# Performance work log

Hardware: AMD Instinct MI355X
Metric: run time of the kernel (lower is better)

## Reference

```python
import jax, jax.numpy as jnp
import numpy as np

HEADS = 8
DIM_HEAD = 64
SCALE = DIM_HEAD ** -0.5


def setup_inputs() -> dict:
    key = jax.random.key(0)
    ks = jax.random.split(key, 6)
    B, N, D = 4, 2048, 512
    inner = HEADS * DIM_HEAD  # 512
    x = jax.random.normal(ks[0], (B, N, D), dtype=jnp.float32)
    centroid_delta = jax.random.normal(ks[1], (B, 3, N, N), dtype=jnp.float32)
    Wqkv = jax.random.normal(ks[2], (D, 3 * inner), dtype=jnp.float32) * (D ** -0.5)
    Wout = jax.random.normal(ks[3], (inner, D), dtype=jnp.float32) * (inner ** -0.5)
    bout = jnp.zeros((D,), dtype=jnp.float32)
    rel_w = jax.random.normal(ks[4], (HEADS, 3), dtype=jnp.float32)
    rel_b = jnp.zeros((HEADS,), dtype=jnp.float32)
    return {"x": x, "centroid_delta": centroid_delta, "Wqkv": Wqkv,
            "Wout": Wout, "bout": bout, "rel_w": rel_w, "rel_b": rel_b}


def reference(x, centroid_delta, Wqkv, Wout, bout, rel_w, rel_b):
    B, N, D = x.shape
    h, d = HEADS, DIM_HEAD
    qkv = x @ Wqkv                      # [B, N, 3*h*d]
    q, k, v = jnp.split(qkv, 3, axis=-1)
    # [B, N, h*d] -> [B, h, N, d]
    reshape = lambda t: t.reshape(B, N, h, d).transpose(0, 2, 1, 3)
    q, k, v = reshape(q), reshape(k), reshape(v)
    dots = jnp.einsum('bhid,bhjd->bhij', q, k) * SCALE  # [B, h, N, N]
    # 1x1 conv: Conv2d(3, heads, 1) on centroid_delta [B, 3, N, N]
    bias = jnp.einsum('hc,bcij->bhij', rel_w, centroid_delta) + rel_b[None, :, None, None]
    attn = jax.nn.softmax(dots + bias, axis=-1)
    out = jnp.einsum('bhij,bhjd->bhid', attn, v)        # [B, h, N, d]
    out = out.transpose(0, 2, 1, 3).reshape(B, N, h * d)
    return out @ Wout + bout
```

## Files before the change

kernel.cpp:

```cpp
#include <hip/hip_runtime.h>
#include <hip/hip_bf16.h>

typedef __bf16 bf16_t;
typedef __bf16 bf16x8 __attribute__((ext_vector_type(8)));
typedef float f32x4 __attribute__((ext_vector_type(4)));

#define SCALE_ 0.125f
#define BATCH 4
#define NSEQ 2048
#define DMODEL 512
#define HEADS 8
#define DHEAD 64
#define QKVN 1536
#define NN ((size_t)NSEQ * NSEQ)

#define BAR() asm volatile("s_waitcnt lgkmcnt(0)\n\ts_barrier" ::: "memory")

__device__ __forceinline__ void gload_lds16(const void* g, void* l) {
  __builtin_amdgcn_global_load_lds((const __attribute__((address_space(1))) void*)g,
                                   (__attribute__((address_space(3))) void*)l, 16, 0, 0);
}

__device__ __forceinline__ f32x4 mfma16(bf16x8 a, bf16x8 b, f32x4 c) {
  return __builtin_amdgcn_mfma_f32_16x16x32_bf16(a, b, c, 0, 0, 0);
}

__global__ __launch_bounds__(256) void cvt_bf16_kernel(const float* __restrict__ in,
                                                       bf16_t* __restrict__ out, int n4) {
  int i = blockIdx.x * 256 + threadIdx.x;
  if (i < n4) {
    float4 v = ((const float4*)in)[i];
    union { bf16_t b[4]; uint2 u; } pk;
    pk.b[0] = (bf16_t)v.x; pk.b[1] = (bf16_t)v.y;
    pk.b[2] = (bf16_t)v.z; pk.b[3] = (bf16_t)v.w;
    ((uint2*)out)[i] = pk.u;
  }
}

__global__ __launch_bounds__(256) void cvt_transpose_kernel(const float* __restrict__ in,
                                                            bf16_t* __restrict__ out, int R, int C) {
  __shared__ float tile[64][65];
  const int r0 = blockIdx.y * 64, c0 = blockIdx.x * 64;
  const int tx = threadIdx.x & 63, tg = threadIdx.x >> 6;
#pragma unroll
  for (int i = 0; i < 16; i++) {
    int rr = tg * 16 + i;
    tile[rr][tx] = in[(size_t)(r0 + rr) * C + c0 + tx];
  }
  __syncthreads();
#pragma unroll
  for (int i = 0; i < 16; i++) {
    int cc = tg * 16 + i;
    out[(size_t)(c0 + cc) * R + r0 + tx] = (bf16_t)tile[tx][cc];
  }
}

template<int BIAS, int OUTF32>
__global__ __launch_bounds__(256) void gemm128_kernel(const bf16_t* __restrict__ A,
    const bf16_t* __restrict__ Bt, void* __restrict__ Cout,
    const float* __restrict__ bias, int M, int N, int K) {
  __shared__ __align__(16) bf16_t As[128 * 64];
  __shared__ __align__(16) bf16_t Bs[128 * 64];
  const int tid = threadIdx.x;
  const int w = tid >> 6, lane = tid & 63, quad = lane >> 4, l16 = lane & 15;
  const int wm = w & 1, wn = w >> 1;
  const int m0 = blockIdx.x * 128, n0 = blockIdx.y * 128;
  f32x4 acc[4][4] = {};
  int srow[4], scg[4];
#pragma unroll
  for (int t = 0; t < 4; t++) {
    int s = (w * 4 + t) * 64 + lane;
    srow[t] = s >> 3;
    scg[t] = (s & 7) ^ (srow[t] & 7);
  }
  for (int k0 = 0; k0 < K; k0 += 64) {
#pragma unroll
    for (int t = 0; t < 4; t++) {
      gload_lds16(&A[(size_t)(m0 + srow[t]) * K + k0 + scg[t] * 8], &As[(w * 4 + t) * 512]);
      gload_lds16(&Bt[(size_t)(n0 + srow[t]) * K + k0 + scg[t] * 8], &Bs[(w * 4 + t) * 512]);
    }
    __syncthreads();
    bf16x8 af[4][2], bfr[4][2];
#pragma unroll
    for (int mt = 0; mt < 4; mt++) {
      int row = wm * 64 + mt * 16 + l16;
#pragma unroll
      for (int kh = 0; kh < 2; kh++)
        af[mt][kh] = *(const bf16x8*)&As[(row * 8 + ((kh * 4 + quad) ^ (row & 7))) * 8];
    }
#pragma unroll
    for (int nt = 0; nt < 4; nt++) {
      int row = wn * 64 + nt * 16 + l16;
#pragma unroll
      for (int kh = 0; kh < 2; kh++)
        bfr[nt][kh] = *(const bf16x8*)&Bs[(row * 8 + ((kh * 4 + quad) ^ (row & 7))) * 8];
    }
#pragma unroll
    for (int mt = 0; mt < 4; mt++)
#pragma unroll
      for (int nt = 0; nt < 4; nt++) {
        acc[mt][nt] = mfma16(af[mt][0], bfr[nt][0], acc[mt][nt]);
        acc[mt][nt] = mfma16(af[mt][1], bfr[nt][1], acc[mt][nt]);
      }
    __syncthreads();
  }
#pragma unroll
  for (int nt = 0; nt < 4; nt++) {
    int col = n0 + wn * 64 + nt * 16 + l16;
    float bv = BIAS ? bias[col] : 0.0f;
#pragma unroll
    for (int mt = 0; mt < 4; mt++) {
#pragma unroll
      for (int rr = 0; rr < 4; rr++) {
        int row = m0 + wm * 64 + mt * 16 + quad * 4 + rr;
        float v = acc[mt][nt][rr] + bv;
        if (OUTF32) ((float*)Cout)[(size_t)row * N + col] = v;
        else        ((bf16_t*)Cout)[(size_t)row * N + col] = (bf16_t)v;
      }
    }
  }
}

__global__ __launch_bounds__(256, 4) void attn_kernel(const bf16_t* __restrict__ qkv,
    const float* __restrict__ cd, const float* __restrict__ rel_w,
    const float* __restrict__ rel_b, bf16_t* __restrict__ ao) {
  __shared__ __align__(16) bf16_t Ks[64][72];
  __shared__ __align__(16) bf16_t Vts[64][72];
  __shared__ __align__(16) bf16_t Ps[64][72];
  const int tid = threadIdx.x;
  const int w = tid >> 6, lane = tid & 63, quad = lane >> 4, l16 = lane & 15;
  const int bid = blockIdx.x;
  const int h = bid >> 7, b = (bid >> 5) & 3, it = bid & 31;

  const size_t qoff = (size_t)(b * NSEQ + it * 64 + w * 16 + l16) * QKVN + h * DHEAD;
  bf16x8 q0 = *(const bf16x8*)&qkv[qoff + quad * 8];
  bf16x8 q1 = *(const bf16x8*)&qkv[qoff + 32 + quad * 8];

  const float rw0 = rel_w[h * 3 + 0], rw1 = rel_w[h * 3 + 1], rw2 = rel_w[h * 3 + 2];
  const float rb = rel_b[h];

  f32x4 o[4] = {};
  float m_r[4], l_r[4];
#pragma unroll
  for (int r = 0; r < 4; r++) { m_r[r] = -1e30f; l_r[r] = 0.0f; }

  const int sr = tid >> 3, sg = tid & 7;
  const size_t kbase = (size_t)b * NSEQ * QKVN + DMODEL + h * DHEAD;

  const int row0 = it * 64 + w * 16 + quad * 4;
  const float* cdp = cd + (size_t)b * 3 * NN + (size_t)row0 * NSEQ + l16;
  float biasr[4][4];
#define LOADBIAS(JT) do { const int jb_ = (JT) * 64;                                   \
  _Pragma("unroll") for (int ct_ = 0; ct_ < 4; ct_++)                                  \
  _Pragma("unroll") for (int r_ = 0; r_ < 4; r_++) {                                   \
    size_t ci_ = (size_t)r_ * NSEQ + jb_ + ct_ * 16;                                   \
    biasr[ct_][r_] = fmaf(rw0, cdp[ci_],                                               \
                     fmaf(rw1, cdp[ci_ + NN], fmaf(rw2, cdp[ci_ + 2 * NN], rb)));      \
  } } while (0)

  uint4 k0r, k1r, v0r, v1r;
  {
    const bf16_t* p = &qkv[kbase + (size_t)sr * QKVN + sg * 8];
    k0r = *(const uint4*)p;               v0r = *(const uint4*)(p + DMODEL);
    k1r = *(const uint4*)(p + 32 * QKVN); v1r = *(const uint4*)(p + 32 * QKVN + DMODEL);
  }
  LOADBIAS(0);

  for (int jt = 0; jt < 32; jt++) {
    *(uint4*)&Ks[sr][sg * 8]      = k0r;
    *(uint4*)&Ks[sr + 32][sg * 8] = k1r;
    {
      union { bf16_t e[8]; uint4 u; } va, vb; va.u = v0r; vb.u = v1r;
      const int pc = sr ^ ((sg & 3) << 3);
#pragma unroll
      for (int e2 = 0; e2 < 8; e2++) {
        Vts[sg * 8 + e2][pc]      = va.e[e2];
        Vts[sg * 8 + e2][pc + 32] = vb.e[e2];
      }
    }
    BAR();

    if (jt < 31) {
      const bf16_t* p = &qkv[kbase + (size_t)((jt + 1) * 64 + sr) * QKVN + sg * 8];
      k0r = *(const uint4*)p;               v0r = *(const uint4*)(p + DMODEL);
      k1r = *(const uint4*)(p + 32 * QKVN); v1r = *(const uint4*)(p + 32 * QKVN + DMODEL);
    }

    f32x4 s[4] = {};
#pragma unroll
    for (int ct = 0; ct < 4; ct++) {
      bf16x8 b0 = *(const bf16x8*)&Ks[ct * 16 + l16][quad * 8];
      bf16x8 b1 = *(const bf16x8*)&Ks[ct * 16 + l16][32 + quad * 8];
      s[ct] = mfma16(q0, b0, s[ct]);
      s[ct] = mfma16(q1, b1, s[ct]);
    }

#pragma unroll
    for (int ct = 0; ct < 4; ct++)
#pragma unroll
      for (int r = 0; r < 4; r++)
        s[ct][r] = s[ct][r] * SCALE_ + biasr[ct][r];
    if (jt < 31) LOADBIAS(jt + 1);

#pragma unroll
    for (int r = 0; r < 4; r++) {
      float mx = fmaxf(fmaxf(s[0][r], s[1][r]), fmaxf(s[2][r], s[3][r]));
#pragma unroll
      for (int off = 8; off >= 1; off >>= 1) mx = fmaxf(mx, __shfl_xor(mx, off, 64));
      float mnew = fmaxf(m_r[r], mx);
      float alpha = __expf(m_r[r] - mnew);
      float rsum = 0.0f;
#pragma unroll
      for (int ct = 0; ct < 4; ct++) {
        float p = __expf(s[ct][r] - mnew);
        s[ct][r] = p; rsum += p;
      }
#pragma unroll
      for (int off = 8; off >= 1; off >>= 1) rsum += __shfl_xor(rsum, off, 64);
      l_r[r] = l_r[r] * alpha + rsum;
      m_r[r] = mnew;
#pragma unroll
      for (int dt = 0; dt < 4; dt++) o[dt][r] *= alpha;
    }

#pragma unroll
    for (int ct = 0; ct < 4; ct++)
#pragma unroll
      for (int rr = 0; rr < 4; rr++)
        Ps[w * 16 + quad * 4 + rr][(ct * 16 + l16) ^ (quad << 3)] = (bf16_t)s[ct][rr];

    const int psw = ((l16 >> 2) & 3) << 3;
    bf16x8 p0 = *(const bf16x8*)&Ps[w * 16 + l16][(quad * 8) ^ psw];
    bf16x8 p1 = *(const bf16x8*)&Ps[w * 16 + l16][32 + ((quad * 8) ^ psw)];
#pragma unroll
    for (int dt = 0; dt < 4; dt++) {
      const int row = dt * 16 + l16;
      const int vsw = ((row >> 3) & 3) << 3;
      bf16x8 v0 = *(const bf16x8*)&Vts[row][(quad * 8) ^ vsw];
      bf16x8 v1 = *(const bf16x8*)&Vts[row][32 + ((quad * 8) ^ vsw)];
      o[dt] = mfma16(p0, v0, o[dt]);
      o[dt] = mfma16(p1, v1, o[dt]);
    }
    BAR();
  }

#pragma unroll
  for (int dt = 0; dt < 4; dt++) {
    int col = h * DHEAD + dt * 16 + l16;
#pragma unroll
    for (int rr = 0; rr < 4; rr++) {
      int row = b * NSEQ + it * 64 + w * 16 + quad * 4 + rr;
      ao[(size_t)row * DMODEL + col] = (bf16_t)(o[dt][rr] / l_r[rr]);
    }
  }
#undef LOADBIAS
}

extern "C" void kernel_launch(void* const* d_in, const int* in_sizes, int n_in,
                              void* d_out, int out_size, void* d_ws, size_t ws_size,
                              hipStream_t stream) {
  const float* x     = (const float*)d_in[0];
  const float* cd    = (const float*)d_in[1];
  const float* Wqkv  = (const float*)d_in[2];
  const float* Wout  = (const float*)d_in[3];
  const float* bout  = (const float*)d_in[4];
  const float* rel_w = (const float*)d_in[5];
  const float* rel_b = (const float*)d_in[6];
  float* out = (float*)d_out;

  char* ws = (char*)d_ws;
  const size_t M = (size_t)BATCH * NSEQ;
  bf16_t* xb    = (bf16_t*)ws;
  bf16_t* WqkvT = (bf16_t*)(ws + 8388608);
  bf16_t* WoutT = (bf16_t*)(ws + 8388608 + 1572864);
  bf16_t* qkv   = (bf16_t*)(ws + 8388608 + 1572864 + 524288);
  bf16_t* ao    = (bf16_t*)(ws + 8388608 + 1572864 + 524288 + 25165824);

  cvt_bf16_kernel<<<(int)(M * DMODEL / 4 / 256), 256, 0, stream>>>(x, xb, (int)(M * DMODEL / 4));
  cvt_transpose_kernel<<<dim3(QKVN / 64, DMODEL / 64), 256, 0, stream>>>(Wqkv, WqkvT, DMODEL, QKVN);
  cvt_transpose_kernel<<<dim3(DMODEL / 64, DMODEL / 64), 256, 0, stream>>>(Wout, WoutT, DMODEL, DMODEL);

  gemm128_kernel<0, 0><<<dim3(M / 128, QKVN / 128), 256, 0, stream>>>(
      xb, WqkvT, (void*)qkv, nullptr, (int)M, QKVN, DMODEL);

  attn_kernel<<<BATCH * 32 * HEADS, 256, 0, stream>>>(qkv, cd, rel_w, rel_b, ao);

  gemm128_kernel<1, 1><<<dim3(M / 128, DMODEL / 128), 256, 0, stream>>>(
      ao, WoutT, (void*)out, bout, (int)M, DMODEL, DMODEL);
}
```

Measured before the change: 443.8 us.

## Pre-transpose V, fold softmax scale into Wqkv, deepen centroid-delta prefetch

Adds a separate kernel that writes V transposed per batch-head, so the attention kernel can store V tiles to LDS with plain vector stores instead of scattered scalar transposing writes. The softmax scale is folded into the Q columns of the weight during conversion. Raw centroid-delta values for the next tile are now prefetched into registers and the bias FMA is used as the MFMA accumulator init. Occupancy is lowered to 3 blocks per SM to fit the larger 48-float prefetch buffer. The trade-offs are an extra kernel launch and extra HBM traffic for vT, and lower occupancy in a kernel that is bound by the centroid-delta stream.

```diff
diff --git a/kernel.cpp b/kernel.cpp
--- a/kernel.cpp
+++ b/kernel.cpp
@@ -5,7 +5,6 @@
 typedef __bf16 bf16x8 __attribute__((ext_vector_type(8)));
 typedef float f32x4 __attribute__((ext_vector_type(4)));
 
-#define SCALE_ 0.125f
 #define BATCH 4
 #define NSEQ 2048
 #define DMODEL 512
@@ -15,6 +14,7 @@
 #define NN ((size_t)NSEQ * NSEQ)
 
 #define BAR() asm volatile("s_waitcnt lgkmcnt(0)\n\ts_barrier" ::: "memory")
+#define PIN() asm volatile("" ::: "memory")
 
 __device__ __forceinline__ void gload_lds16(const void* g, void* l) {
   __builtin_amdgcn_global_load_lds((const __attribute__((address_space(1))) void*)g,
@@ -38,7 +38,8 @@
 }
 
 __global__ __launch_bounds__(256) void cvt_transpose_kernel(const float* __restrict__ in,
-                                                            bf16_t* __restrict__ out, int R, int C) {
+                                                            bf16_t* __restrict__ out, int R, int C,
+                                                            int scaleRows, float sc) {
   __shared__ float tile[64][65];
   const int r0 = blockIdx.y * 64, c0 = blockIdx.x * 64;
   const int tx = threadIdx.x & 63, tg = threadIdx.x >> 6;
@@ -51,7 +52,32 @@
 #pragma unroll
   for (int i = 0; i < 16; i++) {
     int cc = tg * 16 + i;
-    out[(size_t)(c0 + cc) * R + r0 + tx] = (bf16_t)tile[tx][cc];
+    float v = tile[tx][cc];
+    if (c0 + cc < scaleRows) v *= sc;
+    out[(size_t)(c0 + cc) * R + r0 + tx] = (bf16_t)v;
+  }
+}
+
+__global__ __launch_bounds__(256) void vtrans_kernel(const bf16_t* __restrict__ qkv,
+                                                     bf16_t* __restrict__ vT) {
+  __shared__ bf16_t tile[64][72];
+  const int bh = blockIdx.x & 31, jt = blockIdx.x >> 5;
+  const int b = bh >> 3, h = bh & 7;
+  const int tid = threadIdx.x;
+#pragma unroll
+  for (int i = 0; i < 2; i++) {
+    int g = tid * 2 + i, row = g >> 3, gr = g & 7;
+    *(uint4*)&tile[row][gr * 8] =
+        *(const uint4*)&qkv[(size_t)(b * NSEQ + jt * 64 + row) * QKVN + 2 * DMODEL + h * DHEAD + gr * 8];
+  }
+  __syncthreads();
+#pragma unroll
+  for (int i = 0; i < 2; i++) {
+    int g = tid * 2 + i, d = g >> 3, jg = g & 7;
+    union { bf16_t e[8]; uint4 u; } pk;
+#pragma unroll
+    for (int e2 = 0; e2 < 8; e2++) pk.e[e2] = tile[jg * 8 + e2][d];
+    *(uint4*)&vT[(size_t)(bh * 64 + d) * NSEQ + jt * 64 + jg * 8] = pk.u;
   }
 }
 
@@ -121,9 +147,10 @@
   }
 }
 
-__global__ __launch_bounds__(256, 4) void attn_kernel(const bf16_t* __restrict__ qkv,
-    const float* __restrict__ cd, const float* __restrict__ rel_w,
-    const float* __restrict__ rel_b, bf16_t* __restrict__ ao) {
+__global__ __launch_bounds__(256, 3) void attn_kernel(const bf16_t* __restrict__ qkv,
+    const bf16_t* __restrict__ vT, const float* __restrict__ cd,
+    const float* __restrict__ rel_w, const float* __restrict__ rel_b,
+    bf16_t* __restrict__ ao) {
   __shared__ __align__(16) bf16_t Ks[64][72];
   __shared__ __align__(16) bf16_t Vts[64][72];
   __shared__ __align__(16) bf16_t Ps[64][72];
@@ -131,6 +158,7 @@
   const int w = tid >> 6, lane = tid & 63, quad = lane >> 4, l16 = lane & 15;
   const int bid = blockIdx.x;
   const int h = bid >> 7, b = (bid >> 5) & 3, it = bid & 31;
+  const int bh = b * 8 + h;
 
   const size_t qoff = (size_t)(b * NSEQ + it * 64 + w * 16 + l16) * QKVN + h * DHEAD;
   bf16x8 q0 = *(const bf16x8*)&qkv[qoff + quad * 8];
@@ -146,47 +174,63 @@
 
   const int sr = tid >> 3, sg = tid & 7;
   const size_t kbase = (size_t)b * NSEQ * QKVN + DMODEL + h * DHEAD;
+  const bf16_t* vbase = vT + (size_t)(bh * 64) * NSEQ;
 
   const int row0 = it * 64 + w * 16 + quad * 4;
   const float* cdp = cd + (size_t)b * 3 * NN + (size_t)row0 * NSEQ + l16;
-  float biasr[4][4];
-#define LOADBIAS(JT) do { const int jb_ = (JT) * 64;                                   \
-  _Pragma("unroll") for (int ct_ = 0; ct_ < 4; ct_++)                                  \
-  _Pragma("unroll") for (int r_ = 0; r_ < 4; r_++) {                                   \
-    size_t ci_ = (size_t)r_ * NSEQ + jb_ + ct_ * 16;                                   \
-    biasr[ct_][r_] = fmaf(rw0, cdp[ci_],                                               \
-                     fmaf(rw1, cdp[ci_ + NN], fmaf(rw2, cdp[ci_ + 2 * NN], rb)));      \
-  } } while (0)
 
   uint4 k0r, k1r, v0r, v1r;
   {
     const bf16_t* p = &qkv[kbase + (size_t)sr * QKVN + sg * 8];
-    k0r = *(const uint4*)p;               v0r = *(const uint4*)(p + DMODEL);
-    k1r = *(const uint4*)(p + 32 * QKVN); v1r = *(const uint4*)(p + 32 * QKVN + DMODEL);
-  }
-  LOADBIAS(0);
+    k0r = *(const uint4*)p;
+    k1r = *(const uint4*)(p + (size_t)32 * QKVN);
+    v0r = *(const uint4*)&vbase[(size_t)sr * NSEQ + sg * 8];
+    v1r = *(const uint4*)&vbase[(size_t)(sr + 32) * NSEQ + sg * 8];
+  }
+  float cdr[3][4][4];
+#pragma unroll
+  for (int ch = 0; ch < 3; ch++)
+#pragma unroll
+    for (int ct = 0; ct < 4; ct++)
+#pragma unroll
+      for (int r = 0; r < 4; r++)
+        cdr[ch][ct][r] = cdp[ch * NN + (size_t)r * NSEQ + ct * 16];
 
   for (int jt = 0; jt < 32; jt++) {
-    *(uint4*)&Ks[sr][sg * 8]      = k0r;
-    *(uint4*)&Ks[sr + 32][sg * 8] = k1r;
-    {
-      union { bf16_t e[8]; uint4 u; } va, vb; va.u = v0r; vb.u = v1r;
-      const int pc = sr ^ ((sg & 3) << 3);
-#pragma unroll
-      for (int e2 = 0; e2 < 8; e2++) {
-        Vts[sg * 8 + e2][pc]      = va.e[e2];
-        Vts[sg * 8 + e2][pc + 32] = vb.e[e2];
-      }
-    }
+    *(uint4*)&Ks[sr][sg * 8]       = k0r;
+    *(uint4*)&Ks[sr + 32][sg * 8]  = k1r;
+    *(uint4*)&Vts[sr][sg * 8]      = v0r;
+    *(uint4*)&Vts[sr + 32][sg * 8] = v1r;
     BAR();
 
     if (jt < 31) {
       const bf16_t* p = &qkv[kbase + (size_t)((jt + 1) * 64 + sr) * QKVN + sg * 8];
-      k0r = *(const uint4*)p;               v0r = *(const uint4*)(p + DMODEL);
-      k1r = *(const uint4*)(p + 32 * QKVN); v1r = *(const uint4*)(p + 32 * QKVN + DMODEL);
-    }
-
-    f32x4 s[4] = {};
+      k0r = *(const uint4*)p;
+      k1r = *(const uint4*)(p + (size_t)32 * QKVN);
+      v0r = *(const uint4*)&vbase[(size_t)sr * NSEQ + (jt + 1) * 64 + sg * 8];
+      v1r = *(const uint4*)&vbase[(size_t)(sr + 32) * NSEQ + (jt + 1) * 64 + sg * 8];
+    }
+
+    f32x4 s[4];
+#pragma unroll
+    for (int ct = 0; ct < 4; ct++)
+#pragma unroll
+      for (int r = 0; r < 4; r++)
+        s[ct][r] = fmaf(rw0, cdr[0][ct][r],
+                   fmaf(rw1, cdr[1][ct][r], fmaf(rw2, cdr[2][ct][r], rb)));
+
+    if (jt < 31) {
+      const size_t jb = (size_t)(jt + 1) * 64;
+#pragma unroll
+      for (int ch = 0; ch < 3; ch++)
+#pragma unroll
+        for (int ct = 0; ct < 4; ct++)
+#pragma unroll
+          for (int r = 0; r < 4; r++)
+            cdr[ch][ct][r] = cdp[ch * NN + (size_t)r * NSEQ + jb + ct * 16];
+    }
+    PIN();
+
 #pragma unroll
     for (int ct = 0; ct < 4; ct++) {
       bf16x8 b0 = *(const bf16x8*)&Ks[ct * 16 + l16][quad * 8];
@@ -196,13 +240,6 @@
     }
 
 #pragma unroll
-    for (int ct = 0; ct < 4; ct++)
-#pragma unroll
-      for (int r = 0; r < 4; r++)
-        s[ct][r] = s[ct][r] * SCALE_ + biasr[ct][r];
-    if (jt < 31) LOADBIAS(jt + 1);
-
-#pragma unroll
     for (int r = 0; r < 4; r++) {
       float mx = fmaxf(fmaxf(s[0][r], s[1][r]), fmaxf(s[2][r], s[3][r]));
 #pragma unroll
@@ -234,26 +271,26 @@
     bf16x8 p1 = *(const bf16x8*)&Ps[w * 16 + l16][32 + ((quad * 8) ^ psw)];
 #pragma unroll
     for (int dt = 0; dt < 4; dt++) {
-      const int row = dt * 16 + l16;
-      const int vsw = ((row >> 3) & 3) << 3;
-      bf16x8 v0 = *(const bf16x8*)&Vts[row][(quad * 8) ^ vsw];
-      bf16x8 v1 = *(const bf16x8*)&Vts[row][32 + ((quad * 8) ^ vsw)];
+      bf16x8 v0 = *(const bf16x8*)&Vts[dt * 16 + l16][quad * 8];
+      bf16x8 v1 = *(const bf16x8*)&Vts[dt * 16 + l16][32 + quad * 8];
       o[dt] = mfma16(p0, v0, o[dt]);
       o[dt] = mfma16(p1, v1, o[dt]);
     }
     BAR();
   }
 
+  float inv[4];
+#pragma unroll
+  for (int r = 0; r < 4; r++) inv[r] = 1.0f / l_r[r];
 #pragma unroll
   for (int dt = 0; dt < 4; dt++) {
     int col = h * DHEAD + dt * 16 + l16;
 #pragma unroll
     for (int rr = 0; rr < 4; rr++) {
       int row = b * NSEQ + it * 64 + w * 16 + quad * 4 + rr;
-      ao[(size_t)row * DMODEL + col] = (bf16_t)(o[dt][rr] / l_r[rr]);
-    }
-  }
-#undef LOADBIAS
+      ao[(size_t)row * DMODEL + col] = (bf16_t)(o[dt][rr] * inv[rr]);
+    }
+  }
 }
 
 extern "C" void kernel_launch(void* const* d_in, const int* in_sizes, int n_in,
@@ -275,15 +312,20 @@
   bf16_t* WoutT = (bf16_t*)(ws + 8388608 + 1572864);
   bf16_t* qkv   = (bf16_t*)(ws + 8388608 + 1572864 + 524288);
   bf16_t* ao    = (bf16_t*)(ws + 8388608 + 1572864 + 524288 + 25165824);
+  bf16_t* vT    = (bf16_t*)(ws + 8388608 + 1572864 + 524288 + 25165824 + 8388608);
 
   cvt_bf16_kernel<<<(int)(M * DMODEL / 4 / 256), 256, 0, stream>>>(x, xb, (int)(M * DMODEL / 4));
-  cvt_transpose_kernel<<<dim3(QKVN / 64, DMODEL / 64), 256, 0, stream>>>(Wqkv, WqkvT, DMODEL, QKVN);
-  cvt_transpose_kernel<<<dim3(DMODEL / 64, DMODEL / 64), 256, 0, stream>>>(Wout, WoutT, DMODEL, DMODEL);
+  cvt_transpose_kernel<<<dim3(QKVN / 64, DMODEL / 64), 256, 0, stream>>>(
+      Wqkv, WqkvT, DMODEL, QKVN, DMODEL, 0.125f);
+  cvt_transpose_kernel<<<dim3(DMODEL / 64, DMODEL / 64), 256, 0, stream>>>(
+      Wout, WoutT, DMODEL, DMODEL, 0, 1.0f);
 
   gemm128_kernel<0, 0><<<dim3(M / 128, QKVN / 128), 256, 0, stream>>>(
       xb, WqkvT, (void*)qkv, nullptr, (int)M, QKVN, DMODEL);
 
-  attn_kernel<<<BATCH * 32 * HEADS, 256, 0, stream>>>(qkv, cd, rel_w, rel_b, ao);
+  vtrans_kernel<<<1024, 256, 0, stream>>>(qkv, vT);
+
+  attn_kernel<<<BATCH * 32 * HEADS, 256, 0, stream>>>(qkv, vT, cd, rel_w, rel_b, ao);
 
   gemm128_kernel<1, 1><<<dim3(M / 128, DMODEL / 128), 256, 0, stream>>>(
       ao, WoutT, (void*)out, bout, (int)M, DMODEL, DMODEL);
```

After: 477.5 us. 1.08x slower.

## Stage relative-position bias through LDS with coalesced float4 loads and fold scale into Wq

Applied to the files above, without the earlier changes.

The centroid_delta bias tile is now loaded cooperatively with coalesced float4 reads, combined into fp16, written to a shared-memory tile, and read back per lane as the MFMA accumulator's initial value. Before, each lane did strided scalar global loads. The softmax scale is folded into the Q columns of the transposed Wqkv, which removes the per-element multiply. The two weight transposes are merged into one launch, and the final divide becomes a reciprocal multiply. The cost is an extra barrier per tile, more LDS use that may reduce occupancy, and fp16 rounding of the bias.

```diff
diff --git a/kernel.cpp b/kernel.cpp
--- a/kernel.cpp
+++ b/kernel.cpp
@@ -5,7 +5,6 @@
 typedef __bf16 bf16x8 __attribute__((ext_vector_type(8)));
 typedef float f32x4 __attribute__((ext_vector_type(4)));
 
-#define SCALE_ 0.125f
 #define BATCH 4
 #define NSEQ 2048
 #define DMODEL 512
@@ -15,6 +14,7 @@
 #define NN ((size_t)NSEQ * NSEQ)
 
 #define BAR() asm volatile("s_waitcnt lgkmcnt(0)\n\ts_barrier" ::: "memory")
+#define PIN() asm volatile("" ::: "memory")
 
 __device__ __forceinline__ void gload_lds16(const void* g, void* l) {
   __builtin_amdgcn_global_load_lds((const __attribute__((address_space(1))) void*)g,
@@ -37,10 +37,16 @@
   }
 }
 
-__global__ __launch_bounds__(256) void cvt_transpose_kernel(const float* __restrict__ in,
-                                                            bf16_t* __restrict__ out, int R, int C) {
+__global__ __launch_bounds__(256) void cvt_transpose2_kernel(
+    const float* __restrict__ Wqkv, bf16_t* __restrict__ WqkvT,
+    const float* __restrict__ Wout, bf16_t* __restrict__ WoutT) {
   __shared__ float tile[64][65];
+  const float* in; bf16_t* out; int C, scaleRows;
+  if (blockIdx.z == 0) { in = Wqkv; out = WqkvT; C = QKVN; scaleRows = DMODEL; }
+  else                 { in = Wout; out = WoutT; C = DMODEL; scaleRows = 0; }
+  const int R = DMODEL;
   const int r0 = blockIdx.y * 64, c0 = blockIdx.x * 64;
+  if (c0 >= C) return;
   const int tx = threadIdx.x & 63, tg = threadIdx.x >> 6;
 #pragma unroll
   for (int i = 0; i < 16; i++) {
@@ -51,7 +57,9 @@
 #pragma unroll
   for (int i = 0; i < 16; i++) {
     int cc = tg * 16 + i;
-    out[(size_t)(c0 + cc) * R + r0 + tx] = (bf16_t)tile[tx][cc];
+    float v = tile[tx][cc];
+    if (c0 + cc < scaleRows) v *= 0.125f;
+    out[(size_t)(c0 + cc) * R + r0 + tx] = (bf16_t)v;
   }
 }
 
@@ -127,6 +135,7 @@
   __shared__ __align__(16) bf16_t Ks[64][72];
   __shared__ __align__(16) bf16_t Vts[64][72];
   __shared__ __align__(16) bf16_t Ps[64][72];
+  __shared__ __align__(16) _Float16 BiasL[64][68];
   const int tid = threadIdx.x;
   const int w = tid >> 6, lane = tid & 63, quad = lane >> 4, l16 = lane & 15;
   const int bid = blockIdx.x;
@@ -147,24 +156,35 @@
   const int sr = tid >> 3, sg = tid & 7;
   const size_t kbase = (size_t)b * NSEQ * QKVN + DMODEL + h * DHEAD;
 
-  const int row0 = it * 64 + w * 16 + quad * 4;
-  const float* cdp = cd + (size_t)b * 3 * NN + (size_t)row0 * NSEQ + l16;
-  float biasr[4][4];
-#define LOADBIAS(JT) do { const int jb_ = (JT) * 64;                                   \
-  _Pragma("unroll") for (int ct_ = 0; ct_ < 4; ct_++)                                  \
-  _Pragma("unroll") for (int r_ = 0; r_ < 4; r_++) {                                   \
-    size_t ci_ = (size_t)r_ * NSEQ + jb_ + ct_ * 16;                                   \
-    biasr[ct_][r_] = fmaf(rw0, cdp[ci_],                                               \
-                     fmaf(rw1, cdp[ci_ + NN], fmaf(rw2, cdp[ci_ + 2 * NN], rb)));      \
+  const int crow = tid >> 2, ccg = tid & 3;
+  const float* cdt = cd + (size_t)b * 3 * NN + (size_t)(it * 64 + crow) * NSEQ + ccg * 16;
+
+#define COMBINE_WRITE() do {                                                       \
+  _Pragma("unroll") for (int g = 0; g < 4; g++) {                                  \
+    union { _Float16 hh[4]; uint2 u; } pk;                                         \
+    pk.hh[0] = (_Float16)fmaf(rw0, cda[0][g].x, fmaf(rw1, cda[1][g].x, fmaf(rw2, cda[2][g].x, rb))); \
+    pk.hh[1] = (_Float16)fmaf(rw0, cda[0][g].y, fmaf(rw1, cda[1][g].y, fmaf(rw2, cda[2][g].y, rb))); \
+    pk.hh[2] = (_Float16)fmaf(rw0, cda[0][g].z, fmaf(rw1, cda[1][g].z, fmaf(rw2, cda[2][g].z, rb))); \
+    pk.hh[3] = (_Float16)fmaf(rw0, cda[0][g].w, fmaf(rw1, cda[1][g].w, fmaf(rw2, cda[2][g].w, rb))); \
+    *(uint2*)&BiasL[crow][ccg * 16 + g * 4] = pk.u;                                \
   } } while (0)
 
   uint4 k0r, k1r, v0r, v1r;
   {
     const bf16_t* p = &qkv[kbase + (size_t)sr * QKVN + sg * 8];
     k0r = *(const uint4*)p;               v0r = *(const uint4*)(p + DMODEL);
-    k1r = *(const uint4*)(p + 32 * QKVN); v1r = *(const uint4*)(p + 32 * QKVN + DMODEL);
-  }
-  LOADBIAS(0);
+    k1r = *(const uint4*)(p + (size_t)32 * QKVN);
+    v1r = *(const uint4*)(p + (size_t)32 * QKVN + DMODEL);
+  }
+  {
+    float4 cda[3][4];
+#pragma unroll
+    for (int ch = 0; ch < 3; ch++)
+#pragma unroll
+      for (int g = 0; g < 4; g++)
+        cda[ch][g] = *(const float4*)&cdt[ch * NN + g * 4];
+    COMBINE_WRITE();
+  }
 
   for (int jt = 0; jt < 32; jt++) {
     *(uint4*)&Ks[sr][sg * 8]      = k0r;
@@ -180,13 +200,27 @@
     }
     BAR();
 
+    float4 cda[3][4];
     if (jt < 31) {
       const bf16_t* p = &qkv[kbase + (size_t)((jt + 1) * 64 + sr) * QKVN + sg * 8];
       k0r = *(const uint4*)p;               v0r = *(const uint4*)(p + DMODEL);
-      k1r = *(const uint4*)(p + 32 * QKVN); v1r = *(const uint4*)(p + 32 * QKVN + DMODEL);
-    }
-
-    f32x4 s[4] = {};
+      k1r = *(const uint4*)(p + (size_t)32 * QKVN);
+      v1r = *(const uint4*)(p + (size_t)32 * QKVN + DMODEL);
+      const float* cc = cdt + (jt + 1) * 64;
+#pragma unroll
+      for (int ch = 0; ch < 3; ch++)
+#pragma unroll
+        for (int g = 0; g < 4; g++)
+          cda[ch][g] = *(const float4*)&cc[ch * NN + g * 4];
+    }
+    PIN();
+
+    f32x4 s[4];
+#pragma unroll
+    for (int ct = 0; ct < 4; ct++)
+#pragma unroll
+      for (int r = 0; r < 4; r++)
+        s[ct][r] = (float)BiasL[w * 16 + quad * 4 + r][ct * 16 + l16];
 #pragma unroll
     for (int ct = 0; ct < 4; ct++) {
       bf16x8 b0 = *(const bf16x8*)&Ks[ct * 16 + l16][quad * 8];
@@ -194,13 +228,9 @@
       s[ct] = mfma16(q0, b0, s[ct]);
       s[ct] = mfma16(q1, b1, s[ct]);
     }
-
-#pragma unroll
-    for (int ct = 0; ct < 4; ct++)
-#pragma unroll
-      for (int r = 0; r < 4; r++)
-        s[ct][r] = s[ct][r] * SCALE_ + biasr[ct][r];
-    if (jt < 31) LOADBIAS(jt + 1);
+    BAR();
+
+    if (jt < 31) COMBINE_WRITE();
 
 #pragma unroll
     for (int r = 0; r < 4; r++) {
@@ -244,16 +274,19 @@
     BAR();
   }
 
+  float inv[4];
+#pragma unroll
+  for (int r = 0; r < 4; r++) inv[r] = 1.0f / l_r[r];
 #pragma unroll
   for (int dt = 0; dt < 4; dt++) {
     int col = h * DHEAD + dt * 16 + l16;
 #pragma unroll
     for (int rr = 0; rr < 4; rr++) {
       int row = b * NSEQ + it * 64 + w * 16 + quad * 4 + rr;
-      ao[(size_t)row * DMODEL + col] = (bf16_t)(o[dt][rr] / l_r[rr]);
-    }
-  }
-#undef LOADBIAS
+      ao[(size_t)row * DMODEL + col] = (bf16_t)(o[dt][rr] * inv[rr]);
+    }
+  }
+#undef COMBINE_WRITE
 }
 
 extern "C" void kernel_launch(void* const* d_in, const int* in_sizes, int n_in,
@@ -277,8 +310,8 @@
   bf16_t* ao    = (bf16_t*)(ws + 8388608 + 1572864 + 524288 + 25165824);
 
   cvt_bf16_kernel<<<(int)(M * DMODEL / 4 / 256), 256, 0, stream>>>(x, xb, (int)(M * DMODEL / 4));
-  cvt_transpose_kernel<<<dim3(QKVN / 64, DMODEL / 64), 256, 0, stream>>>(Wqkv, WqkvT, DMODEL, QKVN);
-  cvt_transpose_kernel<<<dim3(DMODEL / 64, DMODEL / 64), 256, 0, stream>>>(Wout, WoutT, DMODEL, DMODEL);
+  cvt_transpose2_kernel<<<dim3(QKVN / 64, DMODEL / 64, 2), 256, 0, stream>>>(
+      Wqkv, WqkvT, Wout, WoutT);
 
   gemm128_kernel<0, 0><<<dim3(M / 128, QKVN / 128), 256, 0, stream>>>(
       xb, WqkvT, (void*)qkv, nullptr, (int)M, QKVN, DMODEL);
```

After: 482.0 us. 1.09x slower.
